# Performance work log

Hardware: AMD Instinct MI355X
Metric: run time of the kernel (lower is better)

The kernel has to match this reference:

```python
import jax, jax.numpy as jnp
import numpy as np

B, S, D, H, K = 2, 2048, 1024, 16, 64


def setup_inputs() -> dict:
    key = jax.random.key(0)
    k1, k2, k3 = jax.random.split(key, 3)
    x = jax.random.normal(k1, (B, S, D), dtype=jnp.float32)
    # causal mask: 1 where query can attend to key (key_pos <= pos)
    mask = jnp.tril(jnp.ones((S, S), dtype=jnp.float32))
    W_qkv = jax.random.normal(k2, (D, 3, H, K), dtype=jnp.float32) * 0.02
    b_qkv = jnp.zeros((3, H, K), dtype=jnp.float32)
    W_proj = jax.random.normal(k3, (H, K, D), dtype=jnp.float32) * 0.02
    b_proj = jnp.zeros((D,), dtype=jnp.float32)
    return {"x": x, "mask": mask, "W_qkv": W_qkv, "b_qkv": b_qkv,
            "W_proj": W_proj, "b_proj": b_proj, "layer_idx": 0}


def reference(x, mask, W_qkv, b_qkv, W_proj, b_proj, layer_idx):
    # c_attn: [B,S,D] @ [D,3,H,K] -> [B,S,3,H,K]
    qkv = jnp.einsum('bsd,dthk->bsthk', x, W_qkv) + b_qkv
    q, k, v = qkv[:, :, 0], qkv[:, :, 1], qkv[:, :, 2]  # each [B,S,H,K]
    scale = jax.lax.rsqrt(float(K))  # scale_attn_by_inverse_layer_idx=False
    q = q * scale
    # attn scores over key_size: [B,H,S(pos),S(key_pos)]
    scores = jnp.einsum('bshk,bthk->bhst', q, k)
    scores = scores + (1.0 - mask) * -1e9
    weights = jax.nn.softmax(scores, axis=-1).astype(x.dtype)
    # attn_pdrop = 0.0 -> dropout is identity
    attn_out = jnp.einsum('bhst,bthk->bshk', weights, v)  # [B,S,H,K]
    out = jnp.einsum('bshk,hkd->bsd', attn_out, W_proj) + b_proj
    return out
```

## Files before the change

kernel.cpp:

```cpp
#include <hip/hip_runtime.h>

typedef __bf16 bf16x8 __attribute__((ext_vector_type(8)));
typedef float f32x4 __attribute__((ext_vector_type(4)));
typedef float f32x16 __attribute__((ext_vector_type(16)));
typedef unsigned short u16x8 __attribute__((ext_vector_type(8)));

constexpr int S_LEN = 2048;
constexpr int QKV1  = 2 * 16 * 2048 * 64;
#define LOG2E 1.44269504088896340736f

__device__ inline unsigned short f2bf(float f) {
    __bf16 h = (__bf16)f;
    return __builtin_bit_cast(unsigned short, h);
}

__device__ inline float fexp2(float x) {
    float r;
    asm("v_exp_f32 %0, %1" : "=v"(r) : "v"(x));
    return r;
}

__device__ inline void gll16(const void* g, void* l) {
    __builtin_amdgcn_global_load_lds(
        (const __attribute__((address_space(1))) unsigned int*)g,
        (__attribute__((address_space(3))) unsigned int*)l,
        16, 0, 0);
}

__global__ __launch_bounds__(256) void cvt_f32_bf16(
    const float* __restrict__ src, unsigned short* __restrict__ dst, int n4)
{
    int i = blockIdx.x * 256 + threadIdx.x;
    if (i >= n4) return;
    float4 v = ((const float4*)src)[i];
    ushort4 u;
    u.x = f2bf(v.x); u.y = f2bf(v.y); u.z = f2bf(v.z); u.w = f2bf(v.w);
    ((ushort4*)dst)[i] = u;
}

__global__ __launch_bounds__(256) void transpose_cvt(
    const float* __restrict__ src, unsigned short* __restrict__ dst, int R, int C)
{
    __shared__ float t[32][33];
    const int c0 = blockIdx.x * 32, r0 = blockIdx.y * 32;
    const int tx = threadIdx.x, ty = threadIdx.y;
    #pragma unroll
    for (int i = 0; i < 4; ++i)
        t[ty * 4 + i][tx] = src[(size_t)(r0 + ty * 4 + i) * C + c0 + tx];
    __syncthreads();
    #pragma unroll
    for (int i = 0; i < 4; ++i)
        dst[(size_t)(c0 + ty * 4 + i) * R + r0 + tx] = f2bf(t[tx][ty * 4 + i]);
}

template<int EPI>
__global__ __launch_bounds__(256) void gemm128(
    const unsigned short* __restrict__ A, const unsigned short* __restrict__ Bt,
    const float* __restrict__ bias, void* __restrict__ outp, int M, int N, int K)
{
    __shared__ unsigned short As[2][128 * 32];
    __shared__ unsigned short Bs[2][128 * 32];
    const int tid = threadIdx.x, lane = tid & 63, wid = tid >> 6;
    const int q = lane & 15, g = lane >> 4;
    const int wr = wid >> 1, wc = wid & 1;

    const int nbx = N >> 7;
    const int cpx = gridDim.x >> 3;
    const int bid = blockIdx.x;
    const int swz = (bid & 7) * cpx + (bid >> 3);
    const int m0 = (swz / nbx) * 128, n0 = (swz % nbx) * 128;

    const int srow_in = lane >> 2;
    const int sslot   = (lane & 3) ^ (srow_in & 3);
    auto stage = [&](int buf, int k0) {
        #pragma unroll
        for (int i = 0; i < 2; ++i) {
            int c = wid * 2 + i;
            int row = c * 16 + srow_in;
            gll16(&A [(size_t)(m0 + row) * K + k0 + sslot * 8], &As[buf][c * 512]);
            gll16(&Bt[(size_t)(n0 + row) * K + k0 + sslot * 8], &Bs[buf][c * 512]);
        }
    };

    f32x4 acc[4][4];
    #pragma unroll
    for (int i = 0; i < 4; ++i)
        #pragma unroll
        for (int j = 0; j < 4; ++j) acc[i][j] = (f32x4){0.f, 0.f, 0.f, 0.f};

    const int NSTEP = K >> 5;
    const int rslot = (g ^ (q & 3)) * 8;
    stage(0, 0);
    __syncthreads();
    int cur = 0;

    for (int ks = 0; ks < NSTEP; ++ks) {
        if (ks + 1 < NSTEP) stage(cur ^ 1, (ks + 1) * 32);
        bf16x8 a[4], b[4];
        #pragma unroll
        for (int mi = 0; mi < 4; ++mi)
            a[mi] = *(const bf16x8*)&As[cur][(wr * 64 + mi * 16 + q) * 32 + rslot];
        #pragma unroll
        for (int ni = 0; ni < 4; ++ni)
            b[ni] = *(const bf16x8*)&Bs[cur][(wc * 64 + ni * 16 + q) * 32 + rslot];
        #pragma unroll
        for (int mi = 0; mi < 4; ++mi)
            #pragma unroll
            for (int ni = 0; ni < 4; ++ni)
                acc[mi][ni] = __builtin_amdgcn_mfma_f32_16x16x32_bf16(a[mi], b[ni], acc[mi][ni], 0, 0, 0);
        __syncthreads();
        cur ^= 1;
    }

    #pragma unroll
    for (int mi = 0; mi < 4; ++mi)
        #pragma unroll
        for (int ni = 0; ni < 4; ++ni)
            #pragma unroll
            for (int r = 0; r < 4; ++r) {
                int m = m0 + wr * 64 + mi * 16 + g * 4 + r;
                int n = n0 + wc * 64 + ni * 16 + q;
                float v = acc[mi][ni][r] + bias[n];
                if (EPI == 0) {
                    int t = n >> 10, rem = n & 1023;
                    if (t == 0) v *= 0.125f * LOG2E;
                    int h2 = rem >> 6, kk = rem & 63;
                    int bb = m >> 11, s = m & 2047;
                    size_t off;
                    if (t == 2)
                        off = 2 * (size_t)QKV1 + ((size_t)(bb * 16 + h2) * 64 + kk) * 2048 + s;
                    else
                        off = (size_t)t * QKV1 + ((size_t)(bb * 16 + h2) * 2048 + s) * 64 + kk;
                    ((unsigned short*)outp)[off] = f2bf(v);
                } else {
                    ((float*)outp)[(size_t)m * N + n] = v;
                }
            }
}

__global__ __launch_bounds__(256) void attn_fwd(
    const unsigned short* __restrict__ qkv,
    unsigned short* __restrict__ po, float2* __restrict__ pml)
{
    __shared__ unsigned short Ks[2][64][72];
    __shared__ unsigned short Vs[2][64][72];
    __shared__ float cLds[4][32];
    const int tid = threadIdx.x, lane = tid & 63, wid = tid >> 6;
    const int hi = lane >> 5, lq = lane & 31;
    const int bh = blockIdx.x;
    const int uy = (int)blockIdx.y;
    const int t    = 15 - (uy >> 1);
    const int half = uy & 1;
    const int jb0 = half ? (t + 1) : 0;
    const int jb1 = half ? (2 * t + 2) : (t + 1);
    const unsigned short* Qg = qkv + (size_t)bh * S_LEN * 64;
    const unsigned short* Kg = qkv + (size_t)QKV1 + (size_t)bh * S_LEN * 64;
    const unsigned short* Vt = qkv + 2 * (size_t)QKV1 + (size_t)bh * 64 * S_LEN;

    const int srr = tid >> 3, scc = (tid & 7) * 8;
    u16x8 kr[2], vr[2];
    auto stage_load = [&](int j0) {
        #pragma unroll
        for (int p = 0; p < 2; ++p) {
            kr[p] = *(const u16x8*)&Kg[(size_t)(j0 + srr + p * 32) * 64 + scc];
            vr[p] = *(const u16x8*)&Vt[(size_t)(srr + p * 32) * 2048 + j0 + scc];
        }
    };
    auto stage_write = [&](int b) {
        #pragma unroll
        for (int p = 0; p < 2; ++p) {
            *(u16x8*)&Ks[b][srr + p * 32][scc] = kr[p];
            *(u16x8*)&Vs[b][srr + p * 32][scc] = vr[p];
        }
    };

    const int qbase = t * 128 + wid * 32;
    const int qg = qbase + lq;

    bf16x8 qf[4];
    #pragma unroll
    for (int kc = 0; kc < 4; ++kc)
        qf[kc] = *(const bf16x8*)&Qg[(size_t)qg * 64 + kc * 16 + hi * 8];

    f32x16 z16;
    #pragma unroll
    for (int j = 0; j < 16; ++j) z16[j] = 0.f;

    f32x16 o0 = z16, o1 = z16;
    float m = -1e30f, lr = 0.f;

    stage_load(jb0 * 64);
    stage_write(0);
    int cur = 0;

    for (int jb = jb0; jb < jb1; ++jb) {
        const int j0 = jb * 64;
        if (jb + 1 < jb1) stage_load(j0 + 64);
        __syncthreads();

        if (j0 <= qbase + 31) {
            f32x16 s0, s1;
            __builtin_amdgcn_s_setprio(1);
            {
                bf16x8 k0 = *(const bf16x8*)&Ks[cur][lq][hi * 8];
                bf16x8 k1 = *(const bf16x8*)&Ks[cur][32 + lq][hi * 8];
                s0 = __builtin_amdgcn_mfma_f32_32x32x16_bf16(k0, qf[0], z16, 0, 0, 0);
                s1 = __builtin_amdgcn_mfma_f32_32x32x16_bf16(k1, qf[0], z16, 0, 0, 0);
            }
            #pragma unroll
            for (int kc = 1; kc < 4; ++kc) {
                bf16x8 k0 = *(const bf16x8*)&Ks[cur][lq][kc * 16 + hi * 8];
                bf16x8 k1 = *(const bf16x8*)&Ks[cur][32 + lq][kc * 16 + hi * 8];
                s0 = __builtin_amdgcn_mfma_f32_32x32x16_bf16(k0, qf[kc], s0, 0, 0, 0);
                s1 = __builtin_amdgcn_mfma_f32_32x32x16_bf16(k1, qf[kc], s1, 0, 0, 0);
            }
            __builtin_amdgcn_s_setprio(0);
            if (j0 + 63 > qbase) {
                #pragma unroll
                for (int r = 0; r < 16; ++r) {
                    int kv0 = j0 + (r & 3) + 8 * (r >> 2) + 4 * hi;
                    if (kv0 > qg)      s0[r] = -1e30f;
                    if (kv0 + 32 > qg) s1[r] = -1e30f;
                }
            }
            float tm[8];
            #pragma unroll
            for (int j = 0; j < 8; ++j)
                tm[j] = fmaxf(fmaxf(s0[j], s0[j + 8]), fmaxf(s1[j], s1[j + 8]));
            float pm_loc = fmaxf(fmaxf(fmaxf(tm[0], tm[1]), fmaxf(tm[2], tm[3])),
                                 fmaxf(fmaxf(tm[4], tm[5]), fmaxf(tm[6], tm[7])));
            if (!__all(pm_loc <= m + 8.0f)) {
                float pm = fmaxf(pm_loc, __shfl_xor(pm_loc, 32));
                float mn = fmaxf(m, pm);
                float corr = fexp2(m - mn);
                m = mn; lr *= corr;
                if (lane < 32) cLds[wid][lq] = corr;
                #pragma unroll
                for (int r = 0; r < 16; ++r) {
                    float cq = cLds[wid][(r & 3) + 8 * (r >> 2) + 4 * hi];
                    o0[r] *= cq; o1[r] *= cq;
                }
            }
            float p0[16], p1[16], ts[16];
            #pragma unroll
            for (int j = 0; j < 16; ++j) {
                p0[j] = fexp2(s0[j] - m);
                p1[j] = fexp2(s1[j] - m);
                ts[j] = p0[j] + p1[j];
            }
            #pragma unroll
            for (int w = 8; w > 0; w >>= 1)
                #pragma unroll
                for (int j = 0; j < w; ++j) ts[j] += ts[j + w];
            lr += ts[0];
            int w0[8], w1[8];
            #pragma unroll
            for (int j = 0; j < 8; ++j) {
                asm("v_cvt_pk_bf16_f32 %0, %1, %2" : "=v"(w0[j]) : "v"(p0[2 * j]), "v"(p0[2 * j + 1]));
                asm("v_cvt_pk_bf16_f32 %0, %1, %2" : "=v"(w1[j]) : "v"(p1[2 * j]), "v"(p1[2 * j + 1]));
            }
            bf16x8 pa[4];
            auto mkfrag = [&](const int* w, int base) -> bf16x8 {
                int x0 = __shfl_xor(w[base + 0], 32);
                int x1 = __shfl_xor(w[base + 1], 32);
                int x2 = __shfl_xor(w[base + 2], 32);
                int x3 = __shfl_xor(w[base + 3], 32);
                int4 f;
                f.x = hi ? x2          : w[base + 0];
                f.y = hi ? x3          : w[base + 1];
                f.z = hi ? w[base + 2] : x0;
                f.w = hi ? w[base + 3] : x1;
                return __builtin_bit_cast(bf16x8, f);
            };
            pa[0] = mkfrag(w0, 0);
            pa[1] = mkfrag(w0, 4);
            pa[2] = mkfrag(w1, 0);
            pa[3] = mkfrag(w1, 4);
            __builtin_amdgcn_s_setprio(1);
            #pragma unroll
            for (int kc = 0; kc < 4; ++kc) {
                bf16x8 v0 = *(const bf16x8*)&Vs[cur][lq][kc * 16 + hi * 8];
                bf16x8 v1 = *(const bf16x8*)&Vs[cur][32 + lq][kc * 16 + hi * 8];
                o0 = __builtin_amdgcn_mfma_f32_32x32x16_bf16(pa[kc], v0, o0, 0, 0, 0);
                o1 = __builtin_amdgcn_mfma_f32_32x32x16_bf16(pa[kc], v1, o1, 0, 0, 0);
            }
            __builtin_amdgcn_s_setprio(0);
        }

        if (jb + 1 < jb1) stage_write(cur ^ 1);
        cur ^= 1;
    }

    const int unit = (bh * 16 + t) * 2 + half;
    float lr_full = lr + __shfl_xor(lr, 32);
    if (lane < 32) {
        float2 v; v.x = m; v.y = lr_full;
        pml[unit * 128 + wid * 32 + lq] = v;
    }
    #pragma unroll
    for (int r = 0; r < 16; ++r) {
        int lrow = wid * 32 + (r & 3) + 8 * (r >> 2) + 4 * hi;
        size_t off = ((size_t)unit * 128 + lrow) * 64;
        po[off + lq]      = f2bf(o0[r]);
        po[off + 32 + lq] = f2bf(o1[r]);
    }
}

__global__ __launch_bounds__(256) void attn_combine(
    const unsigned short* __restrict__ po, const float2* __restrict__ pml,
    unsigned short* __restrict__ aout)
{
    const int gid = blockIdx.x * 256 + threadIdx.x;
    const int row = gid >> 2;
    const int cg  = (gid & 3) * 16;
    const int bt = row >> 7, lrow = row & 127;
    const float2 ml0 = pml[(bt * 2 + 0) * 128 + lrow];
    const float2 ml1 = pml[(bt * 2 + 1) * 128 + lrow];
    const float ms = fmaxf(ml0.x, ml1.x);
    float w0 = fexp2(ml0.x - ms), w1 = fexp2(ml1.x - ms);
    const float inv = 1.0f / (ml0.y * w0 + ml1.y * w1);
    w0 *= inv; w1 *= inv;
    const size_t r0 = ((size_t)(bt * 2 + 0) * 128 + lrow) * 64 + cg;
    const size_t r1 = ((size_t)(bt * 2 + 1) * 128 + lrow) * 64 + cg;
    const int bh = bt >> 4, t = bt & 15;
    const int bb = bh >> 4, h = bh & 15;
    const int s = t * 128 + lrow;
    const size_t orow = ((size_t)(bb * 2048 + s)) * 1024 + h * 64 + cg;
    #pragma unroll
    for (int c = 0; c < 2; ++c) {
        u16x8 a = *(const u16x8*)&po[r0 + c * 8];
        u16x8 b = *(const u16x8*)&po[r1 + c * 8];
        u16x8 o;
        #pragma unroll
        for (int e = 0; e < 8; ++e) {
            float fa = __builtin_bit_cast(float, (unsigned)((unsigned short)a[e]) << 16);
            float fb = __builtin_bit_cast(float, (unsigned)((unsigned short)b[e]) << 16);
            o[e] = f2bf(fa * w0 + fb * w1);
        }
        *(u16x8*)&aout[orow + c * 8] = o;
    }
}

extern "C" void kernel_launch(void* const* d_in, const int* in_sizes, int n_in,
                              void* d_out, int out_size, void* d_ws, size_t ws_size,
                              hipStream_t stream) {
    const float* x     = (const float*)d_in[0];
    const float* Wqkv  = (const float*)d_in[2];
    const float* bqkv  = (const float*)d_in[3];
    const float* Wproj = (const float*)d_in[4];
    const float* bproj = (const float*)d_in[5];

    unsigned short* qkvb  = (unsigned short*)d_ws;
    unsigned short* aoutb = qkvb + 3 * (size_t)QKV1;
    float2*         pml   = (float2*)(aoutb + 4096 * 1024);
    unsigned short* Wt   = aoutb;
    unsigned short* Wt2  = qkvb;
    unsigned short* Xbf  = (unsigned short*)d_out;
    unsigned short* po   = (unsigned short*)d_out;

    cvt_f32_bf16<<<4096, 256, 0, stream>>>(x, Xbf, 4096 * 1024 / 4);
    transpose_cvt<<<dim3(96, 32), dim3(32, 8), 0, stream>>>(Wqkv, Wt, 1024, 3072);
    gemm128<0><<<768, 256, 0, stream>>>(Xbf, Wt, bqkv, qkvb, 4096, 3072, 1024);
    attn_fwd<<<dim3(32, 32), 256, 0, stream>>>(qkvb, po, pml);
    attn_combine<<<1024, 256, 0, stream>>>(po, pml, aoutb);
    transpose_cvt<<<dim3(32, 32), dim3(32, 8), 0, stream>>>(Wproj, Wt2, 1024, 1024);
    gemm128<1><<<256, 256, 0, stream>>>(aoutb, Wt2, bproj, d_out, 4096, 1024, 1024);
}
```

Before: 123.0 us.

## Fuse split-attention combine into output projection GEMM A-tile staging

Splits the partial attention outputs into two separate buffers and adds a projection GEMM whose A-tile loader reads both partials and the max/sum stats, then merges them in registers before writing bf16 to LDS. This removes the separate combine kernel and its round trip of the merged attention output through global memory. The fused path runs only when the workspace is large enough, otherwise it falls back to the old two-kernel path. In exchange, A staging now uses synchronous loads plus per-row exp and divide work that is redone for every N-tile block.

New measurement: 133.2 us. 8.2% more time.

```diff
diff --git a/kernel.cpp b/kernel.cpp
--- a/kernel.cpp
+++ b/kernel.cpp
@@ -12,6 +12,9 @@
 __device__ inline unsigned short f2bf(float f) {
     __bf16 h = (__bf16)f;
     return __builtin_bit_cast(unsigned short, h);
+}
+__device__ inline float bf2f(unsigned short u) {
+    return __builtin_bit_cast(float, (unsigned)u << 16);
 }
 
 __device__ inline float fexp2(float x) {
@@ -138,9 +141,114 @@
             }
 }
 
+__global__ __launch_bounds__(256) void gemm128F(
+    const unsigned short* __restrict__ po0, const unsigned short* __restrict__ po1,
+    const float2* __restrict__ pml,
+    const unsigned short* __restrict__ Bt, const float* __restrict__ bias,
+    float* __restrict__ outp, int M, int N, int K)
+{
+    __shared__ unsigned short As[2][128 * 32];
+    __shared__ unsigned short Bs[2][128 * 32];
+    const int tid = threadIdx.x, lane = tid & 63, wid = tid >> 6;
+    const int q = lane & 15, g = lane >> 4;
+    const int wr = wid >> 1, wc = wid & 1;
+
+    const int nbx = N >> 7;
+    const int cpx = gridDim.x >> 3;
+    const int bid = blockIdx.x;
+    const int swz = (bid & 7) * cpx + (bid >> 3);
+    const int m0 = (swz / nbx) * 128, n0 = (swz % nbx) * 128;
+
+    const int srow_in = lane >> 2;
+    const int sslot   = (lane & 3) ^ (srow_in & 3);
+
+    auto stageA = [&](int buf, int k0) {
+        #pragma unroll
+        for (int i = 0; i < 2; ++i) {
+            int c = wid * 2 + i;
+            int row = c * 16 + srow_in;
+            int m = m0 + row;
+            int bbv = m >> 11, s = m & 2047;
+            int tt = s >> 7, lrow = s & 127;
+            int kcol = k0 + sslot * 8;
+            int h2 = kcol >> 6, d = kcol & 63;
+            size_t bt = (size_t)((bbv * 16 + h2) * 16 + tt);
+            size_t prow = (bt * 128 + lrow) * 64 + d;
+            u16x8 a0 = *(const u16x8*)&po0[prow];
+            u16x8 a1 = *(const u16x8*)&po1[prow];
+            float2 ml0 = pml[(bt * 2 + 0) * 128 + lrow];
+            float2 ml1 = pml[(bt * 2 + 1) * 128 + lrow];
+            float ms = fmaxf(ml0.x, ml1.x);
+            float w0 = fexp2(ml0.x - ms), w1 = fexp2(ml1.x - ms);
+            float inv = 1.0f / (ml0.y * w0 + ml1.y * w1);
+            w0 *= inv; w1 *= inv;
+            int outw[4];
+            #pragma unroll
+            for (int e = 0; e < 4; ++e) {
+                float f0 = bf2f((unsigned short)a0[2 * e])     * w0 + bf2f((unsigned short)a1[2 * e])     * w1;
+                float f1 = bf2f((unsigned short)a0[2 * e + 1]) * w0 + bf2f((unsigned short)a1[2 * e + 1]) * w1;
+                asm("v_cvt_pk_bf16_f32 %0, %1, %2" : "=v"(outw[e]) : "v"(f0), "v"(f1));
+            }
+            int4 w4; w4.x = outw[0]; w4.y = outw[1]; w4.z = outw[2]; w4.w = outw[3];
+            *(int4*)&As[buf][c * 512 + lane * 8] = w4;
+        }
+    };
+    auto stageB = [&](int buf, int k0) {
+        #pragma unroll
+        for (int i = 0; i < 2; ++i) {
+            int c = wid * 2 + i;
+            int row = c * 16 + srow_in;
+            gll16(&Bt[(size_t)(n0 + row) * K + k0 + sslot * 8], &Bs[buf][c * 512]);
+        }
+    };
+
+    f32x4 acc[4][4];
+    #pragma unroll
+    for (int i = 0; i < 4; ++i)
+        #pragma unroll
+        for (int j = 0; j < 4; ++j) acc[i][j] = (f32x4){0.f, 0.f, 0.f, 0.f};
+
+    const int NSTEP = K >> 5;
+    const int rslot = (g ^ (q & 3)) * 8;
+    stageA(0, 0);
+    stageB(0, 0);
+    __syncthreads();
+    int cur = 0;
+
+    for (int ks = 0; ks < NSTEP; ++ks) {
+        if (ks + 1 < NSTEP) { stageA(cur ^ 1, (ks + 1) * 32); stageB(cur ^ 1, (ks + 1) * 32); }
+        bf16x8 a[4], b[4];
+        #pragma unroll
+        for (int mi = 0; mi < 4; ++mi)
+            a[mi] = *(const bf16x8*)&As[cur][(wr * 64 + mi * 16 + q) * 32 + rslot];
+        #pragma unroll
+        for (int ni = 0; ni < 4; ++ni)
+            b[ni] = *(const bf16x8*)&Bs[cur][(wc * 64 + ni * 16 + q) * 32 + rslot];
+        #pragma unroll
+        for (int mi = 0; mi < 4; ++mi)
+            #pragma unroll
+            for (int ni = 0; ni < 4; ++ni)
+                acc[mi][ni] = __builtin_amdgcn_mfma_f32_16x16x32_bf16(a[mi], b[ni], acc[mi][ni], 0, 0, 0);
+        __syncthreads();
+        cur ^= 1;
+    }
+
+    #pragma unroll
+    for (int mi = 0; mi < 4; ++mi)
+        #pragma unroll
+        for (int ni = 0; ni < 4; ++ni)
+            #pragma unroll
+            for (int r = 0; r < 4; ++r) {
+                int m = m0 + wr * 64 + mi * 16 + g * 4 + r;
+                int n = n0 + wc * 64 + ni * 16 + q;
+                outp[(size_t)m * N + n] = acc[mi][ni][r] + bias[n];
+            }
+}
+
 __global__ __launch_bounds__(256) void attn_fwd(
     const unsigned short* __restrict__ qkv,
-    unsigned short* __restrict__ po, float2* __restrict__ pml)
+    unsigned short* __restrict__ po0, unsigned short* __restrict__ po1,
+    float2* __restrict__ pml)
 {
     __shared__ unsigned short Ks[2][64][72];
     __shared__ unsigned short Vs[2][64][72];
@@ -291,24 +399,25 @@
         cur ^= 1;
     }
 
-    const int unit = (bh * 16 + t) * 2 + half;
+    const size_t bt = (size_t)bh * 16 + t;
+    unsigned short* pdst = half ? po1 : po0;
     float lr_full = lr + __shfl_xor(lr, 32);
     if (lane < 32) {
         float2 v; v.x = m; v.y = lr_full;
-        pml[unit * 128 + wid * 32 + lq] = v;
+        pml[(bt * 2 + half) * 128 + wid * 32 + lq] = v;
     }
     #pragma unroll
     for (int r = 0; r < 16; ++r) {
         int lrow = wid * 32 + (r & 3) + 8 * (r >> 2) + 4 * hi;
-        size_t off = ((size_t)unit * 128 + lrow) * 64;
-        po[off + lq]      = f2bf(o0[r]);
-        po[off + 32 + lq] = f2bf(o1[r]);
+        size_t off = (bt * 128 + lrow) * 64;
+        pdst[off + lq]      = f2bf(o0[r]);
+        pdst[off + 32 + lq] = f2bf(o1[r]);
     }
 }
 
 __global__ __launch_bounds__(256) void attn_combine(
-    const unsigned short* __restrict__ po, const float2* __restrict__ pml,
-    unsigned short* __restrict__ aout)
+    const unsigned short* __restrict__ po0, const unsigned short* __restrict__ po1,
+    const float2* __restrict__ pml, unsigned short* __restrict__ aout)
 {
     const int gid = blockIdx.x * 256 + threadIdx.x;
     const int row = gid >> 2;
@@ -320,23 +429,19 @@
     float w0 = fexp2(ml0.x - ms), w1 = fexp2(ml1.x - ms);
     const float inv = 1.0f / (ml0.y * w0 + ml1.y * w1);
     w0 *= inv; w1 *= inv;
-    const size_t r0 = ((size_t)(bt * 2 + 0) * 128 + lrow) * 64 + cg;
-    const size_t r1 = ((size_t)(bt * 2 + 1) * 128 + lrow) * 64 + cg;
+    const size_t pr = ((size_t)bt * 128 + lrow) * 64 + cg;
     const int bh = bt >> 4, t = bt & 15;
     const int bb = bh >> 4, h = bh & 15;
     const int s = t * 128 + lrow;
     const size_t orow = ((size_t)(bb * 2048 + s)) * 1024 + h * 64 + cg;
     #pragma unroll
     for (int c = 0; c < 2; ++c) {
-        u16x8 a = *(const u16x8*)&po[r0 + c * 8];
-        u16x8 b = *(const u16x8*)&po[r1 + c * 8];
+        u16x8 a = *(const u16x8*)&po0[pr + c * 8];
+        u16x8 b = *(const u16x8*)&po1[pr + c * 8];
         u16x8 o;
         #pragma unroll
-        for (int e = 0; e < 8; ++e) {
-            float fa = __builtin_bit_cast(float, (unsigned)((unsigned short)a[e]) << 16);
-            float fb = __builtin_bit_cast(float, (unsigned)((unsigned short)b[e]) << 16);
-            o[e] = f2bf(fa * w0 + fb * w1);
-        }
+        for (int e = 0; e < 8; ++e)
+            o[e] = f2bf(bf2f((unsigned short)a[e]) * w0 + bf2f((unsigned short)b[e]) * w1);
         *(u16x8*)&aout[orow + c * 8] = o;
     }
 }
@@ -356,13 +461,29 @@
     unsigned short* Wt   = aoutb;
     unsigned short* Wt2  = qkvb;
     unsigned short* Xbf  = (unsigned short*)d_out;
-    unsigned short* po   = (unsigned short*)d_out;
+
+    const size_t need = 25165824ull + 8388608ull + 1048576ull + 8388608ull;
+    const bool fused = ws_size >= need;
+    unsigned short* po0;
+    unsigned short* po1;
+    if (fused) {
+        po0 = aoutb;
+        po1 = (unsigned short*)((char*)d_ws + 34603008ull);
+    } else {
+        po0 = (unsigned short*)d_out;
+        po1 = (unsigned short*)d_out + 4194304;
+    }
 
     cvt_f32_bf16<<<4096, 256, 0, stream>>>(x, Xbf, 4096 * 1024 / 4);
     transpose_cvt<<<dim3(96, 32), dim3(32, 8), 0, stream>>>(Wqkv, Wt, 1024, 3072);
     gemm128<0><<<768, 256, 0, stream>>>(Xbf, Wt, bqkv, qkvb, 4096, 3072, 1024);
-    attn_fwd<<<dim3(32, 32), 256, 0, stream>>>(qkvb, po, pml);
-    attn_combine<<<1024, 256, 0, stream>>>(po, pml, aoutb);
+    attn_fwd<<<dim3(32, 32), 256, 0, stream>>>(qkvb, po0, po1, pml);
     transpose_cvt<<<dim3(32, 32), dim3(32, 8), 0, stream>>>(Wproj, Wt2, 1024, 1024);
-    gemm128<1><<<256, 256, 0, stream>>>(aoutb, Wt2, bproj, d_out, 4096, 1024, 1024);
-}
+    if (fused) {
+        gemm128F<<<256, 256, 0, stream>>>(po0, po1, pml, Wt2, bproj, (float*)d_out,
+                                          4096, 1024, 1024);
+    } else {
+        attn_combine<<<1024, 256, 0, stream>>>(po0, po1, pml, aoutb);
+        gemm128<1><<<256, 256, 0, stream>>>(aoutb, Wt2, bproj, d_out, 4096, 1024, 1024);
+    }
+}
```
